# Optimization experiments

Measured on AMD Instinct MI355X. Metric: run time of the kernel, lower is better.

Reference implementation:

```python
import jax, jax.numpy as jnp
import numpy as np

# Model dims (init_kwargs): in_channels=hid_channels=128, freq_bins=64, num_heads=8
B, CIN, HID, FREQ, T, H = 4, 128, 128, 64, 512, 8
EPS = 1e-5  # LayerNormalization4D eps


def _conv_act_norm(y, w, b, alpha, gamma, beta):
    """1x1 Conv2d + PReLU + LayerNormalization4D(C,F) on [B, C_in, T, F].
    w: [C_out, C_in], b: [C_out], alpha: scalar PReLU slope,
    gamma/beta: [1, C_out, 1, F]; normalize over (channel, freq) dims."""
    y = jnp.einsum('bctf,oc->botf', y, w) + b[None, :, None, None]
    y = jnp.where(y >= 0, y, alpha * y)  # PReLU (single shared slope)
    mu = jnp.mean(y, axis=(1, 3), keepdims=True)
    var = jnp.mean(jnp.square(y - mu), axis=(1, 3), keepdims=True)
    return (y - mu) / jnp.sqrt(var + EPS) * gamma + beta


def setup_inputs() -> dict:
    key = jax.random.key(0)
    ks = jax.random.split(key, 6)
    s = 0.02
    return {
        'x': jax.random.normal(ks[0], (B, CIN, FREQ, T), jnp.float32),
        'qkv_w': jax.random.normal(ks[1], (3 * HID, CIN), jnp.float32) * s,
        'qkv_b': jnp.zeros((3 * HID,), jnp.float32),
        'qkv_alpha': jnp.float32(0.25),
        'qkv_gamma': jnp.ones((1, 3 * HID, 1, FREQ), jnp.float32),
        'qkv_beta': jnp.zeros((1, 3 * HID, 1, FREQ), jnp.float32),
        'proj_w': jax.random.normal(ks[2], (CIN, CIN), jnp.float32) * s,
        'proj_b': jnp.zeros((CIN,), jnp.float32),
        'proj_alpha': jnp.float32(0.25),
        'proj_gamma': jnp.ones((1, CIN, 1, FREQ), jnp.float32),
        'proj_beta': jnp.zeros((1, CIN, 1, FREQ), jnp.float32),
    }


def reference(x, qkv_w, qkv_b, qkv_alpha, qkv_gamma, qkv_beta,
              proj_w, proj_b, proj_alpha, proj_gamma, proj_beta):
    # x: [B, C, F, T] -> [B, C, T, F]
    xt = jnp.swapaxes(x, -2, -1)
    qkv = _conv_act_norm(xt, qkv_w, qkv_b, qkv_alpha, qkv_gamma, qkv_beta)  # [B, 3*HID, T, F]
    # [B, T, 3*HID, F] -> heads split over flattened (channel, freq) axis
    qkv = jnp.swapaxes(qkv, 1, 2).reshape(B, T, H, -1)
    qkv = jnp.swapaxes(qkv, 1, 2)  # [B, H, T, 3*hd]
    hd = qkv.shape[-1] // 3
    q = qkv[..., :hd]
    k = qkv[..., hd:2 * hd]
    v = qkv[..., 2 * hd:]
    scores = jnp.einsum('bhqd,bhkd->bhqk', q, k) * (hd ** -0.5)
    causal = jnp.triu(jnp.ones((T, T), bool), 1)
    scores = jnp.where(causal[None, None], -jnp.inf, scores)
    attn = jax.nn.softmax(scores, axis=-1)
    ctx = jnp.einsum('bhqk,bhkd->bhqd', attn, v)  # [B, H, T, hd]
    # mimic torch: reshape(B*H, T, hd).transpose(1,2).reshape(B, HID, T, FREQ)
    c = jnp.swapaxes(ctx.reshape(B * H, T, hd), 1, 2).reshape(B, HID, T, FREQ)
    out = _conv_act_norm(c, proj_w, proj_b, proj_alpha, proj_gamma, proj_beta)
    return jnp.swapaxes(out, 2, 3)  # [B, C, F, T]
```

## Files before the change

kernel.cpp:

```cpp
#include <hip/hip_runtime.h>
#include <hip/hip_bf16.h>

#define T_ 512

using sh8 = __attribute__((ext_vector_type(8))) short;
using fx4 = __attribute__((ext_vector_type(4))) float;

__device__ __forceinline__ short bf16r(float x) {
  union { float f; unsigned u; } v; v.f = x;
  unsigned u = v.u;
  u += 0x7fffu + ((u >> 16) & 1u);
  return (short)(u >> 16);
}
__device__ __forceinline__ float b2f(short s) {
  union { float f; unsigned u; } v; v.u = ((unsigned)(unsigned short)s) << 16;
  return v.f;
}
__device__ __forceinline__ fx4 mfma_bf16(sh8 a, sh8 b, fx4 c) {
  return __builtin_amdgcn_mfma_f32_16x16x32_bf16(a, b, c, 0, 0, 0);
}

__global__ __launch_bounds__(256) void k_prep(
    const float* __restrict__ qw, const float* __restrict__ pw,
    const float* __restrict__ gamma, const float* __restrict__ beta,
    short* __restrict__ qwb, short* __restrict__ pwb,
    float* __restrict__ gq, float* __restrict__ bq,
    float* __restrict__ gv, float* __restrict__ bv)
{
  const int i = blockIdx.x * 256 + threadIdx.x;
  if (i < 49152) qwb[i] = bf16r(qw[i]);
  if (i < 16384) pwb[i] = bf16r(pw[i]);
  if (i < 16384) {
    const int sh = i >> 10, dp = i & 1023;
    const int sect = sh >> 3, h = sh & 7;
    const int gi = (h * 48 + sect * 16 + (dp & 15)) * 64 + (dp >> 4);
    gq[i] = gamma[gi]; bq[i] = beta[gi];
  }
  if (i < 8192) {
    const int h = i >> 10, d = i & 1023;
    const int gi = (h * 48 + 32 + (d >> 6)) * 64 + (d & 63);
    gv[i] = gamma[gi]; bv[i] = beta[gi];
  }
}

__global__ __launch_bounds__(256) void k_xt(const float* __restrict__ x,
                                            short* __restrict__ Xb)
{
  const int bid = blockIdx.x;
  const int b = bid >> 8, f = (bid >> 2) & 63, tt = bid & 3;
  const int tid = threadIdx.x;

  __shared__ short Xraw[128 * 128];

  {
    const int tq = (tid & 31) * 4, c0 = tid >> 5;
    const float* xp = x + (((size_t)(b * 128 + c0) * 64 + f) * 512) + tt * 128 + tq;
    #pragma unroll
    for (int p = 0; p < 16; ++p) {
      const int c = c0 + p * 8;
      const float4 fv = *(const float4*)xp;
      xp += 262144;
      short4 o;
      o.x = bf16r(fv.x); o.y = bf16r(fv.y); o.z = bf16r(fv.z); o.w = bf16r(fv.w);
      *(short4*)((char*)Xraw + c * 256 + ((2 * tq) ^ ((c & 7) << 4))) = o;
    }
  }
  __syncthreads();

  short* xb = Xb + (size_t)((b * 64 + f) * 16) * 4096;
  #pragma unroll
  for (int it = 0; it < 8; ++it) {
    const int chunk = tid + it * 256;
    const int c8 = chunk >> 7, tl = chunk & 127;
    sh8 o;
    #pragma unroll
    for (int e = 0; e < 8; ++e)
      o[e] = *((const short*)((const char*)Xraw + (c8 * 8 + e) * 256 + ((2 * tl) ^ (e << 4))));
    *(sh8*)(xb + ((size_t)c8 * 512 + tt * 128 + tl) * 8) = o;
  }
}

__global__ __launch_bounds__(512) void kA_qkv(
    const short* __restrict__ Xb, const short* __restrict__ wb,
    const float* __restrict__ bias, const float* __restrict__ alphap,
    short* __restrict__ Qp, short* __restrict__ Kp, short* __restrict__ Vt,
    float* __restrict__ Pstat)
{
  const int bid = blockIdx.x;
  const int b = bid >> 8, f = (bid >> 2) & 63, tt = bid & 3;
  const int tid = threadIdx.x, lane = tid & 63, w = tid >> 6;

  __shared__ float psum[2048];

  const float alpha = alphap[0];
  fx4 acc[3][8];
  #pragma unroll
  for (int mi = 0; mi < 3; ++mi)
    #pragma unroll
    for (int ni = 0; ni < 8; ++ni) acc[mi][ni] = fx4{0.f, 0.f, 0.f, 0.f};

  const short* xb = Xb + (size_t)((b * 64 + f) * 16) * 4096;

  #pragma unroll
  for (int ks = 0; ks < 4; ++ks) {
    sh8 a[3];
    #pragma unroll
    for (int mi = 0; mi < 3; ++mi) {
      const int o = w * 48 + mi * 16 + (lane & 15);
      a[mi] = *(const sh8*)(wb + o * 128 + ks * 32 + (lane >> 4) * 8);
    }
    #pragma unroll
    for (int ni = 0; ni < 8; ++ni) {
      const sh8 bf = *(const sh8*)(xb + ((size_t)(ks * 4 + (lane >> 4)) * 512 +
                                         tt * 128 + ni * 16 + (lane & 15)) * 8);
      #pragma unroll
      for (int mi = 0; mi < 3; ++mi)
        acc[mi][ni] = mfma_bf16(a[mi], bf, acc[mi][ni]);
    }
  }

  float s0[8], s1[8];
  #pragma unroll
  for (int ni = 0; ni < 8; ++ni) { s0[ni] = 0.f; s1[ni] = 0.f; }
  #pragma unroll
  for (int mi = 0; mi < 3; ++mi)
    #pragma unroll
    for (int r = 0; r < 4; ++r) {
      const int o = w * 48 + mi * 16 + (lane >> 4) * 4 + r;
      const float bo = bias[o];
      #pragma unroll
      for (int ni = 0; ni < 8; ++ni) {
        float v = acc[mi][ni][r] + bo;
        v = (v >= 0.f) ? v : alpha * v;
        acc[mi][ni][r] = v;
        s0[ni] += v; s1[ni] += v * v;
      }
    }
  #pragma unroll
  for (int ni = 0; ni < 8; ++ni) {
    float a0 = s0[ni], a1 = s1[ni];
    a0 += __shfl_down(a0, 32); a1 += __shfl_down(a1, 32);
    a0 += __shfl_down(a0, 16); a1 += __shfl_down(a1, 16);
    if (lane < 16) {
      psum[((w * 8 + ni) * 16 + lane) * 2 + 0] = a0;
      psum[((w * 8 + ni) * 16 + lane) * 2 + 1] = a1;
    }
  }
  __syncthreads();
  if (tid < 256) {
    const int col = tid & 127, s = tid >> 7;
    const int ni = col >> 4, l = col & 15;
    float a0 = 0.f;
    #pragma unroll
    for (int ww = 0; ww < 8; ++ww) a0 += psum[((ww * 8 + ni) * 16 + l) * 2 + s];
    Pstat[(size_t)s * 131072 + (size_t)b * 32768 + (size_t)f * 512 + tt * 128 + col] = a0;
  }

  const int bh = b * 8 + w;
  #pragma unroll
  for (int mi = 0; mi < 2; ++mi) {
    short* dst = mi ? Kp : Qp;
    #pragma unroll
    for (int ni = 0; ni < 8; ++ni) {
      const int t = tt * 128 + ni * 16 + (lane & 15);
      const unsigned lo = (unsigned)(unsigned short)bf16r(acc[mi][ni][0]) |
                          ((unsigned)(unsigned short)bf16r(acc[mi][ni][1]) << 16);
      const unsigned hi = (unsigned)(unsigned short)bf16r(acc[mi][ni][2]) |
                          ((unsigned)(unsigned short)bf16r(acc[mi][ni][3]) << 16);
      uint2 pk; pk.x = lo; pk.y = hi;
      *(uint2*)(dst + ((size_t)bh * 512 + t) * 1024 + f * 16 + (lane >> 4) * 4) = pk;
    }
  }
  #pragma unroll
  for (int ni = 0; ni < 8; ++ni)
    #pragma unroll
    for (int r = 0; r < 4; ++r) {
      const int cl = (lane >> 4) * 4 + r;
      Vt[((size_t)bh * 1024 + cl * 64 + f) * 512 + tt * 128 + ni * 16 + (lane & 15)] =
          bf16r(acc[2][ni][r]);
    }
}

__global__ __launch_bounds__(256) void k_stats(const float* __restrict__ Pstat,
                                               float* __restrict__ MuRs)
{
  const int idx = blockIdx.x * 256 + threadIdx.x;
  const int b = idx >> 9, t = idx & 511;
  float s0 = 0.f, s1 = 0.f;
  for (int f = 0; f < 64; ++f) {
    s0 += Pstat[((size_t)b * 64 + f) * 512 + t];
    s1 += Pstat[131072 + ((size_t)b * 64 + f) * 512 + t];
  }
  const float mu = s0 * (1.f / 24576.f);
  const float var = s1 * (1.f / 24576.f) - mu * mu;
  MuRs[idx * 2] = mu;
  MuRs[idx * 2 + 1] = rsqrtf(var + 1e-5f);
}

__global__ __launch_bounds__(256) void k_qk(
    const short* __restrict__ Qp, const short* __restrict__ Kp,
    const float* __restrict__ MuRs, const float* __restrict__ gq,
    const float* __restrict__ bq, float* __restrict__ S)
{
  const int bid = blockIdx.x;
  const int bh = bid / 10;
  const int j = bid - bh * 10;
  const int qi = (j >= 6) ? 3 : (j >= 3) ? 2 : (j >= 1) ? 1 : 0;
  const int ki = j - qi * (qi + 1) / 2;
  const int b = bh >> 3, h = bh & 7;
  const int tid = threadIdx.x, lane = tid & 63, w = tid >> 6;
  const int wm = w >> 1, wn = w & 1;

  __shared__ short Qs[128 * 128];
  __shared__ short Ks[128 * 128];
  __shared__ float sQ[256], sK[256];

  if (tid < 128) {
    *(float2*)&sQ[tid * 2] = *(const float2*)(MuRs + ((size_t)b * 512 + qi * 128 + tid) * 2);
    *(float2*)&sK[tid * 2] = *(const float2*)(MuRs + ((size_t)b * 512 + ki * 128 + tid) * 2);
  }
  __syncthreads();

  const int op = tid >> 7;
  const int rowslot = (tid >> 4) & 7, unit = tid & 15;
  const short* src = op ? (Kp + ((size_t)bh * 512 + ki * 128) * 1024)
                        : (Qp + ((size_t)bh * 512 + qi * 128) * 1024);
  const float* murs = op ? sK : sQ;
  short* dstl = op ? Ks : Qs;
  const float* gqp = gq + (size_t)(op * 8 + h) * 1024;
  const float* bqp = bq + (size_t)(op * 8 + h) * 1024;

  fx4 acc[4][4];
  #pragma unroll
  for (int mi = 0; mi < 4; ++mi)
    #pragma unroll
    for (int ni = 0; ni < 4; ++ni) acc[mi][ni] = fx4{0.f, 0.f, 0.f, 0.f};

  for (int ks = 0; ks < 8; ++ks) {
    float g8[8], b8[8];
    *(float4*)&g8[0] = *(const float4*)(gqp + ks * 128 + unit * 8);
    *(float4*)&g8[4] = *(const float4*)(gqp + ks * 128 + unit * 8 + 4);
    *(float4*)&b8[0] = *(const float4*)(bqp + ks * 128 + unit * 8);
    *(float4*)&b8[4] = *(const float4*)(bqp + ks * 128 + unit * 8 + 4);
    __syncthreads();
    #pragma unroll
    for (int rit = 0; rit < 16; ++rit) {
      const int row = rit * 8 + rowslot;
      const sh8 v = *(const sh8*)(src + (size_t)row * 1024 + ks * 128 + unit * 8);
      const float mu = murs[row * 2], rs = murs[row * 2 + 1];
      sh8 o;
      #pragma unroll
      for (int e = 0; e < 8; ++e)
        o[e] = bf16r((b2f(v[e]) - mu) * rs * g8[e] + b8[e]);
      *(sh8*)((char*)dstl + row * 256 + ((unit * 16) ^ ((row & 7) << 4))) = o;
    }
    __syncthreads();
    #pragma unroll
    for (int ksub = 0; ksub < 4; ++ksub) {
      sh8 a[4], bb[4];
      #pragma unroll
      for (int mi = 0; mi < 4; ++mi) {
        const int t = wm * 64 + mi * 16 + (lane & 15);
        a[mi] = *(const sh8*)((const char*)Qs + t * 256 +
                ((ksub * 64 + (lane >> 4) * 16) ^ ((t & 7) << 4)));
      }
      #pragma unroll
      for (int ni = 0; ni < 4; ++ni) {
        const int t = wn * 64 + ni * 16 + (lane & 15);
        bb[ni] = *(const sh8*)((const char*)Ks + t * 256 +
                 ((ksub * 64 + (lane >> 4) * 16) ^ ((t & 7) << 4)));
      }
      #pragma unroll
      for (int mi = 0; mi < 4; ++mi)
        #pragma unroll
        for (int ni = 0; ni < 4; ++ni)
          acc[mi][ni] = mfma_bf16(a[mi], bb[ni], acc[mi][ni]);
    }
  }

  float* Sg = S + (size_t)bh * 262144;
  const int q0 = qi * 128 + wm * 64, k0 = ki * 128 + wn * 64;
  #pragma unroll
  for (int mi = 0; mi < 4; ++mi)
    #pragma unroll
    for (int ni = 0; ni < 4; ++ni) {
      const int q = q0 + mi * 16 + (lane >> 4) * 4;
      const int kc = k0 + ni * 16 + (lane & 15);
      #pragma unroll
      for (int r = 0; r < 4; ++r)
        Sg[(size_t)(q + r) * 512 + kc] = acc[mi][ni][r] * 0.03125f;
    }
}

__global__ __launch_bounds__(256) void k_softmax(const float* __restrict__ S,
                                                 short* __restrict__ Pb)
{
  const int row = blockIdx.x * 4 + (threadIdx.x >> 6);
  const int lane = threadIdx.x & 63;
  const int bh = row >> 9, q = row & 511;
  const float* Sr = S + (size_t)bh * 262144 + (size_t)q * 512;
  short* Pr = Pb + (size_t)bh * 262144 + (size_t)q * 512;
  const int n = q + 1;
  float v[8]; float mx = -1e30f;
  #pragma unroll
  for (int i = 0; i < 8; ++i) {
    const int k = lane + i * 64;
    v[i] = (k < n) ? Sr[k] : -1e30f;
    mx = fmaxf(mx, v[i]);
  }
  #pragma unroll
  for (int off = 32; off > 0; off >>= 1) mx = fmaxf(mx, __shfl_xor(mx, off));
  float sum = 0.f;
  #pragma unroll
  for (int i = 0; i < 8; ++i) {
    const float e = (v[i] > -1e29f) ? __expf(v[i] - mx) : 0.f;
    v[i] = e; sum += e;
  }
  #pragma unroll
  for (int off = 32; off > 0; off >>= 1) sum += __shfl_xor(sum, off);
  const float inv = 1.f / sum;
  #pragma unroll
  for (int i = 0; i < 8; ++i) Pr[lane + i * 64] = bf16r(v[i] * inv);
}

__global__ __launch_bounds__(256) void k_pv(
    const short* __restrict__ Pb, const short* __restrict__ Vt,
    const float* __restrict__ MuRs, const float* __restrict__ gv,
    const float* __restrict__ bv, short* __restrict__ Cs)
{
  const int bid = blockIdx.x;
  const int bh = bid >> 5, qi = (bid >> 3) & 3, dt = bid & 7;
  const int b = bh >> 3, h = bh & 7;
  const int tid = threadIdx.x, lane = tid & 63, w = tid >> 6;
  const int wm = w >> 1, wn = w & 1;

  __shared__ char smem[32768];
  short* Ps = (short*)smem;
  short* Vs = (short*)(smem + 16384);
  short* ctile = (short*)smem;

  const short* Pg = Pb + ((size_t)bh * 512 + qi * 128) * 512;
  const short* Vg = Vt + ((size_t)bh * 1024 + dt * 128) * 512;
  const float* gvp = gv + (size_t)h * 1024 + dt * 128;
  const float* bvp = bv + (size_t)h * 1024 + dt * 128;
  const float* mrp = MuRs + (size_t)b * 1024;

  const int rowslot = tid >> 3, unit = tid & 7;

  fx4 acc[4][4];
  #pragma unroll
  for (int mi = 0; mi < 4; ++mi)
    #pragma unroll
    for (int ni = 0; ni < 4; ++ni) acc[mi][ni] = fx4{0.f, 0.f, 0.f, 0.f};

  const int nks = (qi + 1) * 2;
  for (int ks = 0; ks < nks; ++ks) {
    float mr[16];
    *(float4*)&mr[0]  = *(const float4*)(mrp + (ks * 64 + unit * 8) * 2);
    *(float4*)&mr[4]  = *(const float4*)(mrp + (ks * 64 + unit * 8) * 2 + 4);
    *(float4*)&mr[8]  = *(const float4*)(mrp + (ks * 64 + unit * 8) * 2 + 8);
    *(float4*)&mr[12] = *(const float4*)(mrp + (ks * 64 + unit * 8) * 2 + 12);
    __syncthreads();
    #pragma unroll
    for (int rit = 0; rit < 4; ++rit) {
      const int row = rit * 32 + rowslot;
      const sh8 p = *(const sh8*)(Pg + (size_t)row * 512 + ks * 64 + unit * 8);
      *(sh8*)((char*)Ps + row * 128 + ((unit * 16) ^ ((row & 7) << 4))) = p;
      const sh8 vv = *(const sh8*)(Vg + (size_t)row * 512 + ks * 64 + unit * 8);
      const float g = gvp[row], be = bvp[row];
      sh8 o;
      #pragma unroll
      for (int e = 0; e < 8; ++e)
        o[e] = bf16r((b2f(vv[e]) - mr[e * 2]) * mr[e * 2 + 1] * g + be);
      *(sh8*)((char*)Vs + row * 128 + ((unit * 16) ^ ((row & 7) << 4))) = o;
    }
    __syncthreads();
    #pragma unroll
    for (int ksub = 0; ksub < 2; ++ksub) {
      sh8 a[4], bb[4];
      #pragma unroll
      for (int mi = 0; mi < 4; ++mi) {
        const int r2 = wm * 64 + mi * 16 + (lane & 15);
        a[mi] = *(const sh8*)((const char*)Ps + r2 * 128 +
                ((ksub * 64 + (lane >> 4) * 16) ^ ((r2 & 7) << 4)));
      }
      #pragma unroll
      for (int ni = 0; ni < 4; ++ni) {
        const int r2 = wn * 64 + ni * 16 + (lane & 15);
        bb[ni] = *(const sh8*)((const char*)Vs + r2 * 128 +
                 ((ksub * 64 + (lane >> 4) * 16) ^ ((r2 & 7) << 4)));
      }
      #pragma unroll
      for (int mi = 0; mi < 4; ++mi)
        #pragma unroll
        for (int ni = 0; ni < 4; ++ni)
          acc[mi][ni] = mfma_bf16(a[mi], bb[ni], acc[mi][ni]);
    }
  }
  __syncthreads();

  #pragma unroll
  for (int mi = 0; mi < 4; ++mi)
    #pragma unroll
    for (int ni = 0; ni < 4; ++ni) {
      const int ql = wm * 64 + mi * 16 + (lane >> 4) * 4;
      const int dl = wn * 64 + ni * 16 + (lane & 15);
      const int swz = (dl & 7) << 4;
      #pragma unroll
      for (int r = 0; r < 4; ++r)
        ctile[(dl * 256 + ((2 * (ql + r)) ^ swz)) >> 1] = bf16r(acc[mi][ni][r]);
    }
  __syncthreads();

  const int cl_loc = tid >> 7, fq = (tid >> 1) & 63, tg_loc = tid & 1;
  const int C = h * 16 + dt * 2 + cl_loc;
  const int t2 = fq * 8 + qi * 2 + tg_loc;
  const int dl = cl_loc * 64 + fq;
  const int swz = (dl & 7) << 4;
  short* dst = Cs + (((size_t)b * 128 + C) * 512 + t2) * 64;
  #pragma unroll
  for (int jj = 0; jj < 8; ++jj) {
    const sh8 vv = *(const sh8*)((const char*)ctile + dl * 256 + ((tg_loc * 128 + jj * 16) ^ swz));
    *(sh8*)(dst + jj * 8) = vv;
  }
}

__global__ __launch_bounds__(512) void k_proj(
    const short* __restrict__ Cs, const short* __restrict__ wb,
    const float* __restrict__ bias, const float* __restrict__ alphap,
    const float* __restrict__ gamma, const float* __restrict__ beta,
    short* __restrict__ Otmpb)
{
  const int bid = blockIdx.x;
  const int b = bid >> 9, t2 = bid & 511;
  const int tid = threadIdx.x, lane = tid & 63, w = tid >> 6;

  __shared__ short Xs[64 * 128];
  __shared__ float red[18];

  {
    const int rowslot = tid >> 3, unit = tid & 7;
    #pragma unroll
    for (int rit = 0; rit < 2; ++rit) {
      const int C = rit * 64 + rowslot;
      const sh8 vv = *(const sh8*)(Cs + (((size_t)b * 128 + C) * 512 + t2) * 64 + unit * 8);
      #pragma unroll
      for (int jj = 0; jj < 8; ++jj) {
        const int f2 = unit * 8 + jj;
        *((short*)((char*)Xs + f2 * 256 + ((2 * C) ^ ((f2 & 7) << 4)))) = vv[jj];
      }
    }
  }
  __syncthreads();

  const float alpha = alphap[0];
  fx4 acc[4];
  #pragma unroll
  for (int ni = 0; ni < 4; ++ni) acc[ni] = fx4{0.f, 0.f, 0.f, 0.f};

  #pragma unroll
  for (int ks = 0; ks < 4; ++ks) {
    const int o = w * 16 + (lane & 15);
    const sh8 a = *(const sh8*)(wb + o * 128 + ks * 32 + (lane >> 4) * 8);
    #pragma unroll
    for (int ni = 0; ni < 4; ++ni) {
      const int f2 = ni * 16 + (lane & 15);
      const sh8 bf = *(const sh8*)((const char*)Xs + f2 * 256 +
                     ((ks * 64 + (lane >> 4) * 16) ^ ((f2 & 7) << 4)));
      acc[ni] = mfma_bf16(a, bf, acc[ni]);
    }
  }

  float s0 = 0.f, s1 = 0.f;
  const int ob = w * 16 + (lane >> 4) * 4;
  #pragma unroll
  for (int ni = 0; ni < 4; ++ni)
    #pragma unroll
    for (int r = 0; r < 4; ++r) {
      float v = acc[ni][r] + bias[ob + r];
      v = (v >= 0.f) ? v : alpha * v;
      acc[ni][r] = v;
      s0 += v; s1 += v * v;
    }
  #pragma unroll
  for (int off = 32; off > 0; off >>= 1) { s0 += __shfl_down(s0, off); s1 += __shfl_down(s1, off); }
  if (lane == 0) { red[w * 2] = s0; red[w * 2 + 1] = s1; }
  __syncthreads();
  if (tid == 0) {
    float a0 = 0.f, a1 = 0.f;
    for (int i2 = 0; i2 < 8; ++i2) { a0 += red[2 * i2]; a1 += red[2 * i2 + 1]; }
    const float mu = a0 / 8192.f;
    const float var = a1 / 8192.f - mu * mu;
    red[16] = mu; red[17] = rsqrtf(var + 1e-5f);
  }
  __syncthreads();
  const float mu = red[16], rstd = red[17];

  #pragma unroll
  for (int ni = 0; ni < 4; ++ni) {
    const int f2 = ni * 16 + (lane & 15);
    #pragma unroll
    for (int r = 0; r < 4; ++r) {
      const int o = ob + r;
      const float zz = (acc[ni][r] - mu) * rstd * gamma[o * 64 + f2] + beta[o * 64 + f2];
      Otmpb[(((size_t)b * 128 + o) * 512 + t2) * 64 + f2] = bf16r(zz);
    }
  }
}

__global__ __launch_bounds__(256) void k_trans(const short* __restrict__ Otmpb,
                                               float* __restrict__ out)
{
  const int bid = blockIdx.x;
  const int bo = bid >> 3, tt8 = bid & 7;
  const int t20 = tt8 * 64;
  const int tid = threadIdx.x;
  __shared__ float Ltr[64 * 68];

  {
    const int t2l = tid >> 2, u = tid & 3;
    const short* srow = Otmpb + ((size_t)bo * 512 + t20 + t2l) * 64 + u * 16;
    const sh8 v0 = *(const sh8*)(srow);
    const sh8 v1 = *(const sh8*)(srow + 8);
    #pragma unroll
    for (int e = 0; e < 8; ++e) {
      Ltr[(u * 16 + e) * 68 + t2l]     = b2f(v0[e]);
      Ltr[(u * 16 + 8 + e) * 68 + t2l] = b2f(v1[e]);
    }
  }
  __syncthreads();
  {
    const int f2 = tid >> 2, u = tid & 3;
    float* dst = out + ((size_t)bo * 64 + f2) * 512 + t20 + u * 16;
    #pragma unroll
    for (int k = 0; k < 4; ++k)
      *(float4*)(dst + k * 4) = *(const float4*)&Ltr[f2 * 68 + u * 16 + k * 4];
  }
}

extern "C" void kernel_launch(void* const* d_in, const int* in_sizes, int n_in,
                              void* d_out, int out_size, void* d_ws, size_t ws_size,
                              hipStream_t stream) {
  (void)in_sizes; (void)n_in; (void)out_size;
  const float* x          = (const float*)d_in[0];
  const float* qkv_w      = (const float*)d_in[1];
  const float* qkv_b      = (const float*)d_in[2];
  const float* qkv_alpha  = (const float*)d_in[3];
  const float* qkv_gamma  = (const float*)d_in[4];
  const float* qkv_beta   = (const float*)d_in[5];
  const float* proj_w     = (const float*)d_in[6];
  const float* proj_b     = (const float*)d_in[7];
  const float* proj_alpha = (const float*)d_in[8];
  const float* proj_gamma = (const float*)d_in[9];
  const float* proj_beta  = (const float*)d_in[10];
  float* out = (float*)d_out;

  char* ws = (char*)d_ws;
  short* Qp   = (short*)(ws + 0);
  short* Kp   = (short*)(ws + 33554432);
  short* Vt   = (short*)(ws + 67108864);
  short* Xb   = (short*)(ws + 100663296);
  float* S    = (float*)(ws + 100663296);
  short* Pb   = (short*)(ws + 134217728);
  float* MuRs = (float*)(ws + 150994944);
  float* gq   = (float*)(ws + 151011328);
  float* bq   = (float*)(ws + 151076864);
  float* gv   = (float*)(ws + 151142400);
  float* bv   = (float*)(ws + 151175168);
  short* Cs    = (short*)(ws + 0);
  short* Otmpb = (short*)(ws + 33554432);
  short* qwb  = (short*)(ws + 167772160);
  short* pwb  = (short*)(ws + 167870464);
  float* Pstat = (float*)d_out;
  if (ws_size < 167903232u) return;

  k_prep<<<192, 256, 0, stream>>>(qkv_w, proj_w, qkv_gamma, qkv_beta,
                                  qwb, pwb, gq, bq, gv, bv);
  k_xt<<<1024, 256, 0, stream>>>(x, Xb);
  kA_qkv<<<1024, 512, 0, stream>>>(Xb, qwb, qkv_b, qkv_alpha, Qp, Kp, Vt, Pstat);
  k_stats<<<8, 256, 0, stream>>>(Pstat, MuRs);
  k_qk<<<320, 256, 0, stream>>>(Qp, Kp, MuRs, gq, bq, S);
  k_softmax<<<4096, 256, 0, stream>>>(S, Pb);
  k_pv<<<1024, 256, 0, stream>>>(Pb, Vt, MuRs, gv, bv, Cs);
  k_proj<<<2048, 512, 0, stream>>>(Cs, pwb, proj_b, proj_alpha, proj_gamma, proj_beta, Otmpb);
  k_trans<<<4096, 256, 0, stream>>>(Otmpb, out);
}
```

Baseline: 252.9 us.

## Fuse QK, softmax and PV into flash-style kernel with algebraic LayerNorm folding

Replaces the separate QK-score, softmax and PV kernels with one flash-attention kernel that uses an online softmax, so the full score matrix and probability matrix no longer round-trip through global memory. The LayerNorm of Q, K and V is folded algebraically: per-row statistics and gamma/beta cross terms are precomputed in the qkv and stats kernels, and scores and outputs are corrected with rank-one terms. This avoids normalizing Q, K and V tiles inside the attention loop. It adds extra partial-sum traffic through the Pstat buffer, heavier register use (32 output accumulators per lane), and V operands read straight from global memory rather than staged in LDS.

```diff
diff --git a/kernel.cpp b/kernel.cpp
--- a/kernel.cpp
+++ b/kernel.cpp
@@ -25,8 +25,40 @@
     const float* __restrict__ gamma, const float* __restrict__ beta,
     short* __restrict__ qwb, short* __restrict__ pwb,
     float* __restrict__ gq, float* __restrict__ bq,
-    float* __restrict__ gv, float* __restrict__ bv)
+    float* __restrict__ gv, float* __restrict__ bv,
+    float* __restrict__ HC)
 {
+  __shared__ float cred[4][4];
+  if (blockIdx.x >= 192) {
+    const int h = blockIdx.x - 192;
+    float c0 = 0.f, c1 = 0.f, c2 = 0.f, c3 = 0.f;
+    #pragma unroll
+    for (int e = 0; e < 4; ++e) {
+      const int dp = threadIdx.x * 4 + e;
+      const int cl = dp & 15, fq = dp >> 4;
+      const float gqv = gamma[(h * 48 + cl) * 64 + fq];
+      const float gkv = gamma[(h * 48 + 16 + cl) * 64 + fq];
+      const float bqv = beta[(h * 48 + cl) * 64 + fq];
+      const float bkv = beta[(h * 48 + 16 + cl) * 64 + fq];
+      c0 += gqv * gkv; c1 += gqv * bkv; c2 += gkv * bqv; c3 += bqv * bkv;
+    }
+    #pragma unroll
+    for (int off = 32; off > 0; off >>= 1) {
+      c0 += __shfl_down(c0, off); c1 += __shfl_down(c1, off);
+      c2 += __shfl_down(c2, off); c3 += __shfl_down(c3, off);
+    }
+    if ((threadIdx.x & 63) == 0) {
+      cred[threadIdx.x >> 6][0] = c0; cred[threadIdx.x >> 6][1] = c1;
+      cred[threadIdx.x >> 6][2] = c2; cred[threadIdx.x >> 6][3] = c3;
+    }
+    __syncthreads();
+    if (threadIdx.x < 4) {
+      float s = 0.f;
+      for (int k2 = 0; k2 < 4; ++k2) s += cred[k2][threadIdx.x];
+      HC[h * 4 + threadIdx.x] = s;
+    }
+    return;
+  }
   const int i = blockIdx.x * 256 + threadIdx.x;
   if (i < 49152) qwb[i] = bf16r(qw[i]);
   if (i < 16384) pwb[i] = bf16r(pw[i]);
@@ -83,6 +115,7 @@
 __global__ __launch_bounds__(512) void kA_qkv(
     const short* __restrict__ Xb, const short* __restrict__ wb,
     const float* __restrict__ bias, const float* __restrict__ alphap,
+    const float* __restrict__ gq, const float* __restrict__ bq,
     short* __restrict__ Qp, short* __restrict__ Kp, short* __restrict__ Vt,
     float* __restrict__ Pstat)
 {
@@ -90,9 +123,8 @@
   const int b = bid >> 8, f = (bid >> 2) & 63, tt = bid & 3;
   const int tid = threadIdx.x, lane = tid & 63, w = tid >> 6;
 
-  __shared__ float psum[2048];
-
-  const float alpha = alphap[0];
+  __shared__ float psum[8 * 8 * 16 * 6];
+
   fx4 acc[3][8];
   #pragma unroll
   for (int mi = 0; mi < 3; ++mi)
@@ -119,41 +151,61 @@
     }
   }
 
-  float s0[8], s1[8];
-  #pragma unroll
-  for (int ni = 0; ni < 8; ++ni) { s0[ni] = 0.f; s1[ni] = 0.f; }
-  #pragma unroll
-  for (int mi = 0; mi < 3; ++mi)
-    #pragma unroll
-    for (int r = 0; r < 4; ++r) {
-      const int o = w * 48 + mi * 16 + (lane >> 4) * 4 + r;
-      const float bo = bias[o];
-      #pragma unroll
-      for (int ni = 0; ni < 8; ++ni) {
-        float v = acc[mi][ni][r] + bo;
+  float gqq[4], gqk[4], bqq[4], bqk[4];
+  #pragma unroll
+  for (int r = 0; r < 4; ++r) {
+    const int dp = f * 16 + (lane >> 4) * 4 + r;
+    gqq[r] = gq[w * 1024 + dp];
+    gqk[r] = gq[(8 + w) * 1024 + dp];
+    bqq[r] = bq[w * 1024 + dp];
+    bqk[r] = bq[(8 + w) * 1024 + dp];
+  }
+
+  const float alpha = alphap[0];
+  #pragma unroll
+  for (int ni = 0; ni < 8; ++ni) {
+    float t0 = 0.f, t1 = 0.f, taq = 0.f, tuq = 0.f, tak = 0.f, tuk = 0.f;
+    #pragma unroll
+    for (int mi = 0; mi < 3; ++mi)
+      #pragma unroll
+      for (int r = 0; r < 4; ++r) {
+        const int o = w * 48 + mi * 16 + (lane >> 4) * 4 + r;
+        float v = acc[mi][ni][r] + bias[o];
         v = (v >= 0.f) ? v : alpha * v;
         acc[mi][ni][r] = v;
-        s0[ni] += v; s1[ni] += v * v;
-      }
-    }
-  #pragma unroll
-  for (int ni = 0; ni < 8; ++ni) {
-    float a0 = s0[ni], a1 = s1[ni];
-    a0 += __shfl_down(a0, 32); a1 += __shfl_down(a1, 32);
-    a0 += __shfl_down(a0, 16); a1 += __shfl_down(a1, 16);
+        t0 += v; t1 += v * v;
+        if (mi == 0) { const float qt = v * gqq[r]; taq += qt * gqk[r]; tuq += qt * bqk[r]; }
+        if (mi == 1) { const float kt = v * gqk[r]; tak += kt * gqq[r]; tuk += kt * bqq[r]; }
+      }
+    t0 += __shfl_down(t0, 32); t1 += __shfl_down(t1, 32);
+    taq += __shfl_down(taq, 32); tuq += __shfl_down(tuq, 32);
+    tak += __shfl_down(tak, 32); tuk += __shfl_down(tuk, 32);
+    t0 += __shfl_down(t0, 16); t1 += __shfl_down(t1, 16);
+    taq += __shfl_down(taq, 16); tuq += __shfl_down(tuq, 16);
+    tak += __shfl_down(tak, 16); tuk += __shfl_down(tuk, 16);
     if (lane < 16) {
-      psum[((w * 8 + ni) * 16 + lane) * 2 + 0] = a0;
-      psum[((w * 8 + ni) * 16 + lane) * 2 + 1] = a1;
-    }
-  }
-  __syncthreads();
+      float* ps = &psum[((w * 8 + ni) * 16 + lane) * 6];
+      ps[0] = t0; ps[1] = t1; ps[2] = taq; ps[3] = tuq; ps[4] = tak; ps[5] = tuk;
+    }
+  }
+  __syncthreads();
+
   if (tid < 256) {
     const int col = tid & 127, s = tid >> 7;
     const int ni = col >> 4, l = col & 15;
     float a0 = 0.f;
     #pragma unroll
-    for (int ww = 0; ww < 8; ++ww) a0 += psum[((ww * 8 + ni) * 16 + l) * 2 + s];
+    for (int ww = 0; ww < 8; ++ww) a0 += psum[((ww * 8 + ni) * 16 + l) * 6 + s];
     Pstat[(size_t)s * 131072 + (size_t)b * 32768 + (size_t)f * 512 + tt * 128 + col] = a0;
+  }
+  #pragma unroll
+  for (int p = 0; p < 8; ++p) {
+    const int idx = p * 512 + tid;
+    const int col = idx & 127, wc = idx >> 7;
+    const int ww = wc >> 2, ch = wc & 3;
+    const int ni = col >> 4, l = col & 15;
+    Pstat[(size_t)(2 + ww * 4 + ch) * 131072 + (size_t)b * 32768 +
+          (size_t)f * 512 + tt * 128 + col] = psum[((ww * 8 + ni) * 16 + l) * 6 + 2 + ch];
   }
 
   const int bh = b * 8 + w;
@@ -163,10 +215,14 @@
     #pragma unroll
     for (int ni = 0; ni < 8; ++ni) {
       const int t = tt * 128 + ni * 16 + (lane & 15);
-      const unsigned lo = (unsigned)(unsigned short)bf16r(acc[mi][ni][0]) |
-                          ((unsigned)(unsigned short)bf16r(acc[mi][ni][1]) << 16);
-      const unsigned hi = (unsigned)(unsigned short)bf16r(acc[mi][ni][2]) |
-                          ((unsigned)(unsigned short)bf16r(acc[mi][ni][3]) << 16);
+      float v0 = acc[mi][ni][0] * (mi == 0 ? gqq[0] : gqk[0]);
+      float v1 = acc[mi][ni][1] * (mi == 0 ? gqq[1] : gqk[1]);
+      float v2 = acc[mi][ni][2] * (mi == 0 ? gqq[2] : gqk[2]);
+      float v3 = acc[mi][ni][3] * (mi == 0 ? gqq[3] : gqk[3]);
+      const unsigned lo = (unsigned)(unsigned short)bf16r(v0) |
+                          ((unsigned)(unsigned short)bf16r(v1) << 16);
+      const unsigned hi = (unsigned)(unsigned short)bf16r(v2) |
+                          ((unsigned)(unsigned short)bf16r(v3) << 16);
       uint2 pk; pk.x = lo; pk.y = hi;
       *(uint2*)(dst + ((size_t)bh * 512 + t) * 1024 + f * 16 + (lane >> 4) * 4) = pk;
     }
@@ -182,246 +238,216 @@
 }
 
 __global__ __launch_bounds__(256) void k_stats(const float* __restrict__ Pstat,
-                                               float* __restrict__ MuRs)
+                                               const float* __restrict__ HC,
+                                               float* __restrict__ RowB)
 {
   const int idx = blockIdx.x * 256 + threadIdx.x;
-  const int b = idx >> 9, t = idx & 511;
-  float s0 = 0.f, s1 = 0.f;
-  for (int f = 0; f < 64; ++f) {
-    s0 += Pstat[((size_t)b * 64 + f) * 512 + t];
-    s1 += Pstat[131072 + ((size_t)b * 64 + f) * 512 + t];
+  const int b = idx >> 12, h = (idx >> 9) & 7, t = idx & 511;
+  const float* P0 = Pstat + (size_t)b * 32768 + t;
+  float s0 = 0.f, s1 = 0.f, aq = 0.f, uq = 0.f, ak = 0.f, uk = 0.f;
+  for (int fq = 0; fq < 64; ++fq) {
+    const size_t o = (size_t)fq * 512;
+    s0 += P0[o];
+    s1 += P0[(size_t)131072 + o];
+    aq += P0[(size_t)(2 + h * 4 + 0) * 131072 + o];
+    uq += P0[(size_t)(2 + h * 4 + 1) * 131072 + o];
+    ak += P0[(size_t)(2 + h * 4 + 2) * 131072 + o];
+    uk += P0[(size_t)(2 + h * 4 + 3) * 131072 + o];
   }
   const float mu = s0 * (1.f / 24576.f);
   const float var = s1 * (1.f / 24576.f) - mu * mu;
-  MuRs[idx * 2] = mu;
-  MuRs[idx * 2 + 1] = rsqrtf(var + 1e-5f);
-}
-
-__global__ __launch_bounds__(256) void k_qk(
+  const float rs = rsqrtf(var + 1e-5f);
+  const float rm = rs * mu;
+  float* o8 = RowB + ((size_t)(b * 8 + h) * 512 + t) * 8;
+  o8[0] = rs;
+  o8[1] = rm;
+  o8[2] = rs * aq;
+  o8[3] = rs * uq - rm * HC[h * 4 + 1];
+  o8[4] = rs * ak;
+  o8[5] = rs * uk - rm * HC[h * 4 + 2];
+  o8[6] = 0.f; o8[7] = 0.f;
+}
+
+__global__ __launch_bounds__(256, 2) void k_flash(
     const short* __restrict__ Qp, const short* __restrict__ Kp,
-    const float* __restrict__ MuRs, const float* __restrict__ gq,
-    const float* __restrict__ bq, float* __restrict__ S)
+    const short* __restrict__ Vt, const float* __restrict__ RowB,
+    const float* __restrict__ gvt, const float* __restrict__ bvt,
+    const float* __restrict__ HC, short* __restrict__ Cs)
 {
   const int bid = blockIdx.x;
-  const int bh = bid / 10;
-  const int j = bid - bh * 10;
-  const int qi = (j >= 6) ? 3 : (j >= 3) ? 2 : (j >= 1) ? 1 : 0;
-  const int ki = j - qi * (qi + 1) / 2;
+  const int qx = bid >> 6;
+  const int qi = (qx < 4) ? qx : (11 - qx);
+  const int dh = (bid >> 5) & 1, bh = bid & 31;
   const int b = bh >> 3, h = bh & 7;
   const int tid = threadIdx.x, lane = tid & 63, w = tid >> 6;
-  const int wm = w >> 1, wn = w & 1;
-
-  __shared__ short Qs[128 * 128];
-  __shared__ short Ks[128 * 128];
-  __shared__ float sQ[256], sK[256];
-
-  if (tid < 128) {
-    *(float2*)&sQ[tid * 2] = *(const float2*)(MuRs + ((size_t)b * 512 + qi * 128 + tid) * 2);
-    *(float2*)&sK[tid * 2] = *(const float2*)(MuRs + ((size_t)b * 512 + ki * 128 + tid) * 2);
-  }
-  __syncthreads();
-
-  const int op = tid >> 7;
-  const int rowslot = (tid >> 4) & 7, unit = tid & 15;
-  const short* src = op ? (Kp + ((size_t)bh * 512 + ki * 128) * 1024)
-                        : (Qp + ((size_t)bh * 512 + qi * 128) * 1024);
-  const float* murs = op ? sK : sQ;
-  short* dstl = op ? Ks : Qs;
-  const float* gqp = gq + (size_t)(op * 8 + h) * 1024;
-  const float* bqp = bq + (size_t)(op * 8 + h) * 1024;
-
-  fx4 acc[4][4];
-  #pragma unroll
-  for (int mi = 0; mi < 4; ++mi)
-    #pragma unroll
-    for (int ni = 0; ni < 4; ++ni) acc[mi][ni] = fx4{0.f, 0.f, 0.f, 0.f};
-
-  for (int ks = 0; ks < 8; ++ks) {
-    float g8[8], b8[8];
-    *(float4*)&g8[0] = *(const float4*)(gqp + ks * 128 + unit * 8);
-    *(float4*)&g8[4] = *(const float4*)(gqp + ks * 128 + unit * 8 + 4);
-    *(float4*)&b8[0] = *(const float4*)(bqp + ks * 128 + unit * 8);
-    *(float4*)&b8[4] = *(const float4*)(bqp + ks * 128 + unit * 8 + 4);
+
+  __shared__ __align__(16) char smem[65536];
+  float4* kb = (float4*)(smem + 49152);
+  float4* qb = (float4*)(smem + 51200);
+
+  const float Ggg = HC[h * 4 + 0], Bbb = HC[h * 4 + 3];
+
+  if (tid < 64)
+    qb[tid] = *(const float4*)(RowB + ((size_t)(b * 8 + h) * 512 + qi * 64 + tid) * 8);
+
+  const short* Qg = Qp + ((size_t)bh * 512 + qi * 64) * 1024;
+  const short* Kg = Kp + (size_t)bh * 512 * 1024;
+  const short* Vg = Vt + (size_t)bh * 1024 * 512;
+
+  fx4 oacc[32];
+  #pragma unroll
+  for (int nd = 0; nd < 32; ++nd) oacc[nd] = fx4{0.f, 0.f, 0.f, 0.f};
+  float mq[4], lq[4], saq[4];
+  #pragma unroll
+  for (int i = 0; i < 4; ++i) { mq[i] = -1e30f; lq[i] = 0.f; saq[i] = 0.f; }
+
+  const int KT = (qi >> 1) + 1;
+  for (int kt = 0; kt < KT; ++kt) {
     __syncthreads();
-    #pragma unroll
-    for (int rit = 0; rit < 16; ++rit) {
-      const int row = rit * 8 + rowslot;
-      const sh8 v = *(const sh8*)(src + (size_t)row * 1024 + ks * 128 + unit * 8);
-      const float mu = murs[row * 2], rs = murs[row * 2 + 1];
-      sh8 o;
-      #pragma unroll
-      for (int e = 0; e < 8; ++e)
-        o[e] = bf16r((b2f(v[e]) - mu) * rs * g8[e] + b8[e]);
-      *(sh8*)((char*)dstl + row * 256 + ((unit * 16) ^ ((row & 7) << 4))) = o;
+    if (tid < 128) {
+      const float* rb = RowB + ((size_t)(b * 8 + h) * 512 + kt * 128 + tid) * 8;
+      const float4 lo = *(const float4*)rb;
+      const float4 hi = *(const float4*)(rb + 4);
+      kb[tid] = float4{lo.x, lo.y, hi.x, hi.y};
+    }
+
+    fx4 sacc[8];
+    #pragma unroll
+    for (int ni = 0; ni < 8; ++ni) sacc[ni] = fx4{0.f, 0.f, 0.f, 0.f};
+
+    for (int ks = 0; ks < 8; ++ks) {
+      __syncthreads();
+      #pragma unroll
+      for (int p = 0; p < 4; ++p) {
+        const int idx = tid + p * 256;
+        const int row = idx >> 4, c = idx & 15;
+        const sh8 v = *(const sh8*)(Qg + (size_t)row * 1024 + ks * 128 + c * 8);
+        *(sh8*)(smem + row * 256 + ((c * 16) ^ ((row & 7) << 4))) = v;
+      }
+      #pragma unroll
+      for (int p = 0; p < 8; ++p) {
+        const int idx = tid + p * 256;
+        const int row = idx >> 4, c = idx & 15;
+        const sh8 v = *(const sh8*)(Kg + (size_t)(kt * 128 + row) * 1024 + ks * 128 + c * 8);
+        *(sh8*)(smem + 16384 + row * 256 + ((c * 16) ^ ((row & 7) << 4))) = v;
+      }
+      __syncthreads();
+      #pragma unroll
+      for (int kk = 0; kk < 4; ++kk) {
+        const int arow = w * 16 + (lane & 15);
+        const sh8 a = *(const sh8*)(smem + arow * 256 +
+                      (((kk * 32 + (lane >> 4) * 8) * 2) ^ ((arow & 7) << 4)));
+        #pragma unroll
+        for (int ni = 0; ni < 8; ++ni) {
+          const int brow = ni * 16 + (lane & 15);
+          const sh8 bbf = *(const sh8*)(smem + 16384 + brow * 256 +
+                          (((kk * 32 + (lane >> 4) * 8) * 2) ^ ((brow & 7) << 4)));
+          sacc[ni] = mfma_bf16(a, bbf, sacc[ni]);
+        }
+      }
     }
     __syncthreads();
-    #pragma unroll
-    for (int ksub = 0; ksub < 4; ++ksub) {
-      sh8 a[4], bb[4];
-      #pragma unroll
-      for (int mi = 0; mi < 4; ++mi) {
-        const int t = wm * 64 + mi * 16 + (lane & 15);
-        a[mi] = *(const sh8*)((const char*)Qs + t * 256 +
-                ((ksub * 64 + (lane >> 4) * 16) ^ ((t & 7) << 4)));
-      }
-      #pragma unroll
-      for (int ni = 0; ni < 4; ++ni) {
-        const int t = wn * 64 + ni * 16 + (lane & 15);
-        bb[ni] = *(const sh8*)((const char*)Ks + t * 256 +
-                 ((ksub * 64 + (lane >> 4) * 16) ^ ((t & 7) << 4)));
-      }
-      #pragma unroll
-      for (int mi = 0; mi < 4; ++mi)
-        #pragma unroll
-        for (int ni = 0; ni < 4; ++ni)
-          acc[mi][ni] = mfma_bf16(a[mi], bb[ni], acc[mi][ni]);
-    }
-  }
-
-  float* Sg = S + (size_t)bh * 262144;
-  const int q0 = qi * 128 + wm * 64, k0 = ki * 128 + wn * 64;
-  #pragma unroll
-  for (int mi = 0; mi < 4; ++mi)
-    #pragma unroll
-    for (int ni = 0; ni < 4; ++ni) {
-      const int q = q0 + mi * 16 + (lane >> 4) * 4;
-      const int kc = k0 + ni * 16 + (lane & 15);
-      #pragma unroll
-      for (int r = 0; r < 4; ++r)
-        Sg[(size_t)(q + r) * 512 + kc] = acc[mi][ni][r] * 0.03125f;
-    }
-}
-
-__global__ __launch_bounds__(256) void k_softmax(const float* __restrict__ S,
-                                                 short* __restrict__ Pb)
-{
-  const int row = blockIdx.x * 4 + (threadIdx.x >> 6);
-  const int lane = threadIdx.x & 63;
-  const int bh = row >> 9, q = row & 511;
-  const float* Sr = S + (size_t)bh * 262144 + (size_t)q * 512;
-  short* Pr = Pb + (size_t)bh * 262144 + (size_t)q * 512;
-  const int n = q + 1;
-  float v[8]; float mx = -1e30f;
-  #pragma unroll
-  for (int i = 0; i < 8; ++i) {
-    const int k = lane + i * 64;
-    v[i] = (k < n) ? Sr[k] : -1e30f;
-    mx = fmaxf(mx, v[i]);
-  }
-  #pragma unroll
-  for (int off = 32; off > 0; off >>= 1) mx = fmaxf(mx, __shfl_xor(mx, off));
-  float sum = 0.f;
-  #pragma unroll
-  for (int i = 0; i < 8; ++i) {
-    const float e = (v[i] > -1e29f) ? __expf(v[i] - mx) : 0.f;
-    v[i] = e; sum += e;
-  }
-  #pragma unroll
-  for (int off = 32; off > 0; off >>= 1) sum += __shfl_xor(sum, off);
-  const float inv = 1.f / sum;
-  #pragma unroll
-  for (int i = 0; i < 8; ++i) Pr[lane + i * 64] = bf16r(v[i] * inv);
-}
-
-__global__ __launch_bounds__(256) void k_pv(
-    const short* __restrict__ Pb, const short* __restrict__ Vt,
-    const float* __restrict__ MuRs, const float* __restrict__ gv,
-    const float* __restrict__ bv, short* __restrict__ Cs)
-{
-  const int bid = blockIdx.x;
-  const int bh = bid >> 5, qi = (bid >> 3) & 3, dt = bid & 7;
-  const int b = bh >> 3, h = bh & 7;
-  const int tid = threadIdx.x, lane = tid & 63, w = tid >> 6;
-  const int wm = w >> 1, wn = w & 1;
-
-  __shared__ char smem[32768];
-  short* Ps = (short*)smem;
-  short* Vs = (short*)(smem + 16384);
-  short* ctile = (short*)smem;
-
-  const short* Pg = Pb + ((size_t)bh * 512 + qi * 128) * 512;
-  const short* Vg = Vt + ((size_t)bh * 1024 + dt * 128) * 512;
-  const float* gvp = gv + (size_t)h * 1024 + dt * 128;
-  const float* bvp = bv + (size_t)h * 1024 + dt * 128;
-  const float* mrp = MuRs + (size_t)b * 1024;
-
-  const int rowslot = tid >> 3, unit = tid & 7;
-
-  fx4 acc[4][4];
-  #pragma unroll
-  for (int mi = 0; mi < 4; ++mi)
-    #pragma unroll
-    for (int ni = 0; ni < 4; ++ni) acc[mi][ni] = fx4{0.f, 0.f, 0.f, 0.f};
-
-  const int nks = (qi + 1) * 2;
-  for (int ks = 0; ks < nks; ++ks) {
-    float mr[16];
-    *(float4*)&mr[0]  = *(const float4*)(mrp + (ks * 64 + unit * 8) * 2);
-    *(float4*)&mr[4]  = *(const float4*)(mrp + (ks * 64 + unit * 8) * 2 + 4);
-    *(float4*)&mr[8]  = *(const float4*)(mrp + (ks * 64 + unit * 8) * 2 + 8);
-    *(float4*)&mr[12] = *(const float4*)(mrp + (ks * 64 + unit * 8) * 2 + 12);
+
+    float pm[4];
+    #pragma unroll
+    for (int r = 0; r < 4; ++r) pm[r] = -3e30f;
+
+    #pragma unroll
+    for (int ni = 0; ni < 8; ++ni) {
+      const int kl = ni * 16 + (lane & 15);
+      const float4 kv = kb[kl];
+      #pragma unroll
+      for (int r = 0; r < 4; ++r) {
+        const int ql = w * 16 + (lane >> 4) * 4 + r;
+        const float4 qv = qb[ql];
+        float s = sacc[ni][r];
+        s = qv.x * kv.x * s - qv.z * kv.y - qv.y * kv.z + (qv.y * kv.y) * Ggg
+            + qv.w + kv.w + Bbb;
+        s *= 0.03125f;
+        if (kt * 128 + kl > qi * 64 + ql) s = -3e30f;
+        sacc[ni][r] = s;
+        pm[r] = fmaxf(pm[r], s);
+      }
+    }
+    #pragma unroll
+    for (int r = 0; r < 4; ++r) {
+      float v = pm[r];
+      v = fmaxf(v, __shfl_xor(v, 1)); v = fmaxf(v, __shfl_xor(v, 2));
+      v = fmaxf(v, __shfl_xor(v, 4)); v = fmaxf(v, __shfl_xor(v, 8));
+      const float mn = fmaxf(mq[r], v);
+      const float fsc = __expf(mq[r] - mn);
+      mq[r] = mn;
+      lq[r] *= fsc; saq[r] *= fsc;
+      #pragma unroll
+      for (int nd = 0; nd < 32; ++nd) oacc[nd][r] *= fsc;
+    }
+    #pragma unroll
+    for (int ni = 0; ni < 8; ++ni) {
+      const int kl = ni * 16 + (lane & 15);
+      const float4 kv = kb[kl];
+      #pragma unroll
+      for (int r = 0; r < 4; ++r) {
+        const int ql = w * 16 + (lane >> 4) * 4 + r;
+        const float p = __expf(sacc[ni][r] - mq[r]);
+        lq[r] += p; saq[r] += p * kv.y;
+        *((short*)(smem + ql * 256 + ((kl * 2) ^ ((ql & 7) << 4)))) = bf16r(p * kv.x);
+      }
+    }
     __syncthreads();
-    #pragma unroll
-    for (int rit = 0; rit < 4; ++rit) {
-      const int row = rit * 32 + rowslot;
-      const sh8 p = *(const sh8*)(Pg + (size_t)row * 512 + ks * 64 + unit * 8);
-      *(sh8*)((char*)Ps + row * 128 + ((unit * 16) ^ ((row & 7) << 4))) = p;
-      const sh8 vv = *(const sh8*)(Vg + (size_t)row * 512 + ks * 64 + unit * 8);
-      const float g = gvp[row], be = bvp[row];
-      sh8 o;
-      #pragma unroll
-      for (int e = 0; e < 8; ++e)
-        o[e] = bf16r((b2f(vv[e]) - mr[e * 2]) * mr[e * 2 + 1] * g + be);
-      *(sh8*)((char*)Vs + row * 128 + ((unit * 16) ^ ((row & 7) << 4))) = o;
-    }
-    __syncthreads();
-    #pragma unroll
-    for (int ksub = 0; ksub < 2; ++ksub) {
-      sh8 a[4], bb[4];
-      #pragma unroll
-      for (int mi = 0; mi < 4; ++mi) {
-        const int r2 = wm * 64 + mi * 16 + (lane & 15);
-        a[mi] = *(const sh8*)((const char*)Ps + r2 * 128 +
-                ((ksub * 64 + (lane >> 4) * 16) ^ ((r2 & 7) << 4)));
-      }
-      #pragma unroll
-      for (int ni = 0; ni < 4; ++ni) {
-        const int r2 = wn * 64 + ni * 16 + (lane & 15);
-        bb[ni] = *(const sh8*)((const char*)Vs + r2 * 128 +
-                 ((ksub * 64 + (lane >> 4) * 16) ^ ((r2 & 7) << 4)));
-      }
-      #pragma unroll
-      for (int mi = 0; mi < 4; ++mi)
-        #pragma unroll
-        for (int ni = 0; ni < 4; ++ni)
-          acc[mi][ni] = mfma_bf16(a[mi], bb[ni], acc[mi][ni]);
-    }
-  }
-  __syncthreads();
-
-  #pragma unroll
-  for (int mi = 0; mi < 4; ++mi)
-    #pragma unroll
-    for (int ni = 0; ni < 4; ++ni) {
-      const int ql = wm * 64 + mi * 16 + (lane >> 4) * 4;
-      const int dl = wn * 64 + ni * 16 + (lane & 15);
-      const int swz = (dl & 7) << 4;
-      #pragma unroll
-      for (int r = 0; r < 4; ++r)
-        ctile[(dl * 256 + ((2 * (ql + r)) ^ swz)) >> 1] = bf16r(acc[mi][ni][r]);
-    }
-  __syncthreads();
-
-  const int cl_loc = tid >> 7, fq = (tid >> 1) & 63, tg_loc = tid & 1;
-  const int C = h * 16 + dt * 2 + cl_loc;
-  const int t2 = fq * 8 + qi * 2 + tg_loc;
-  const int dl = cl_loc * 64 + fq;
-  const int swz = (dl & 7) << 4;
-  short* dst = Cs + (((size_t)b * 128 + C) * 512 + t2) * 64;
-  #pragma unroll
-  for (int jj = 0; jj < 8; ++jj) {
-    const sh8 vv = *(const sh8*)((const char*)ctile + dl * 256 + ((tg_loc * 128 + jj * 16) ^ swz));
-    *(sh8*)(dst + jj * 8) = vv;
+
+    #pragma unroll
+    for (int kk = 0; kk < 4; ++kk) {
+      const int arow = w * 16 + (lane & 15);
+      const sh8 a2 = *(const sh8*)(smem + arow * 256 +
+                     (((kk * 32 + (lane >> 4) * 8) * 2) ^ ((arow & 7) << 4)));
+      #pragma unroll
+      for (int nd = 0; nd < 32; ++nd) {
+        const sh8 vb = *(const sh8*)(Vg +
+            ((size_t)(dh * 512 + nd * 16 + (lane & 15))) * 512 +
+            kt * 128 + kk * 32 + (lane >> 4) * 8);
+        oacc[nd] = mfma_bf16(a2, vb, oacc[nd]);
+      }
+    }
+  }
+
+  #pragma unroll
+  for (int r = 0; r < 4; ++r) {
+    float L = lq[r], S = saq[r];
+    #pragma unroll
+    for (int off = 1; off < 16; off <<= 1) {
+      L += __shfl_xor(L, off); S += __shfl_xor(S, off);
+    }
+    lq[r] = 1.0f / L; saq[r] = S;
+  }
+  __syncthreads();
+
+  #pragma unroll
+  for (int nd = 0; nd < 32; ++nd) {
+    const int dl = nd * 16 + (lane & 15);
+    const float gvv = gvt[h * 1024 + dh * 512 + dl];
+    const float bvv = bvt[h * 1024 + dh * 512 + dl];
+    const int swz = (dl & 7) << 4;
+    #pragma unroll
+    for (int r = 0; r < 4; ++r) {
+      const int ql = w * 16 + (lane >> 4) * 4 + r;
+      const float o = gvv * (oacc[nd][r] - saq[r]) * lq[r] + bvv;
+      *((short*)(smem + dl * 128 + ((ql * 2) ^ swz))) = bf16r(o);
+    }
+  }
+  __syncthreads();
+
+  #pragma unroll
+  for (int rr = 0; rr < 2; ++rr) {
+    const int dl = rr * 256 + tid;
+    const int C = h * 16 + dh * 8 + (dl >> 6);
+    const int t2 = (dl & 63) * 8 + qi;
+    short* dst = Cs + (((size_t)b * 128 + C) * 512 + t2) * 64;
+    const int swz = (dl & 7) << 4;
+    #pragma unroll
+    for (int j = 0; j < 8; ++j) {
+      const sh8 vv = *(const sh8*)(smem + dl * 128 + ((j * 16) ^ swz));
+      *(sh8*)(dst + j * 8) = vv;
+    }
   }
 }
 
@@ -557,31 +583,29 @@
 
   char* ws = (char*)d_ws;
   short* Qp   = (short*)(ws + 0);
+  short* Otmpb= (short*)(ws + 0);
   short* Kp   = (short*)(ws + 33554432);
   short* Vt   = (short*)(ws + 67108864);
   short* Xb   = (short*)(ws + 100663296);
-  float* S    = (float*)(ws + 100663296);
-  short* Pb   = (short*)(ws + 134217728);
-  float* MuRs = (float*)(ws + 150994944);
-  float* gq   = (float*)(ws + 151011328);
-  float* bq   = (float*)(ws + 151076864);
-  float* gv   = (float*)(ws + 151142400);
-  float* bv   = (float*)(ws + 151175168);
-  short* Cs    = (short*)(ws + 0);
-  short* Otmpb = (short*)(ws + 33554432);
+  short* Cs   = (short*)(ws + 100663296);
+  float* RowB = (float*)(ws + 134217728);
+  float* gq   = (float*)(ws + 134742016);
+  float* bq   = (float*)(ws + 134807552);
+  float* gv   = (float*)(ws + 134873088);
+  float* bv   = (float*)(ws + 134905856);
+  float* HC   = (float*)(ws + 134938624);
   short* qwb  = (short*)(ws + 167772160);
   short* pwb  = (short*)(ws + 167870464);
   float* Pstat = (float*)d_out;
   if (ws_size < 167903232u) return;
 
-  k_prep<<<192, 256, 0, stream>>>(qkv_w, proj_w, qkv_gamma, qkv_beta,
-                                  qwb, pwb, gq, bq, gv, bv);
+  k_prep<<<200, 256, 0, stream>>>(qkv_w, proj_w, qkv_gamma, qkv_beta,
+                                  qwb, pwb, gq, bq, gv, bv, HC);
   k_xt<<<1024, 256, 0, stream>>>(x, Xb);
-  kA_qkv<<<1024, 512, 0, stream>>>(Xb, qwb, qkv_b, qkv_alpha, Qp, Kp, Vt, Pstat);
-  k_stats<<<8, 256, 0, stream>>>(Pstat, MuRs);
-  k_qk<<<320, 256, 0, stream>>>(Qp, Kp, MuRs, gq, bq, S);
-  k_softmax<<<4096, 256, 0, stream>>>(S, Pb);
-  k_pv<<<1024, 256, 0, stream>>>(Pb, Vt, MuRs, gv, bv, Cs);
+  kA_qkv<<<1024, 512, 0, stream>>>(Xb, qwb, qkv_b, qkv_alpha, gq, bq,
+                                   Qp, Kp, Vt, Pstat);
+  k_stats<<<64, 256, 0, stream>>>(Pstat, HC, RowB);
+  k_flash<<<512, 256, 0, stream>>>(Qp, Kp, Vt, RowB, gv, bv, HC, Cs);
   k_proj<<<2048, 512, 0, stream>>>(Cs, pwb, proj_b, proj_alpha, proj_gamma, proj_beta, Otmpb);
   k_trans<<<4096, 256, 0, stream>>>(Otmpb, out);
 }
```

After: 651.6 us. 158% more time.
